# Optimization experiments

Measured on AMD Instinct MI355X. Metric: run time of the kernel, lower is better.

## Reference

```python
import jax, jax.numpy as jnp
import numpy as np

A, B, OBS, ACT, H, G = 8, 4096, 512, 64, 1024, 64
N, E = 10000, 40000
NODE, GH, NTYPES, AEMB = 32, 64, 8, 16


def _ln(x, g, b, eps=1e-5):
    m = jnp.mean(x, -1, keepdims=True)
    v = jnp.mean((x - m) ** 2, -1, keepdims=True)
    return (x - m) * jax.lax.rsqrt(v + eps) * g + b


def _neigh_mean(h, edges, n):
    # undirected mean aggregation: each dependency edge contributes both ways
    s, d = edges[:, 0], edges[:, 1]
    agg = jnp.zeros((n, h.shape[-1]), h.dtype).at[d].add(h[s]).at[s].add(h[d])
    deg = jnp.zeros((n,), h.dtype).at[d].add(1.0).at[s].add(1.0)
    return agg / jnp.maximum(deg, 1.0)[:, None]


def setup_inputs() -> dict:
    key = jax.random.key(0)
    ks = jax.random.split(key, 32)
    f32 = jnp.float32

    def w(k, i, o):
        return (jax.random.normal(k, (i, o), f32) / np.sqrt(i)).astype(f32)

    d = {}
    d["observations"] = jax.random.normal(ks[0], (A, B, OBS), f32)
    d["node_types"] = jax.random.randint(ks[1], (N,), 0, NTYPES)
    d["node_agents"] = jax.random.randint(ks[2], (N,), 0, A)
    d["edges"] = jax.random.randint(ks[3], (E, 2), 0, N)
    # graph encoder params
    d["type_embed"] = (jax.random.normal(ks[4], (NTYPES, NODE), f32) * 0.02).astype(f32)
    d["gagent_embed"] = (jax.random.normal(ks[5], (A, NODE), f32) * 0.02).astype(f32)
    d["W_l0"] = w(ks[6], 2 * NODE, GH); d["b_l0"] = jnp.zeros((GH,), f32)
    d["g_l0"] = jnp.ones((GH,), f32);   d["be_l0"] = jnp.zeros((GH,), f32)
    d["W_l1"] = w(ks[7], GH + GH, G);   d["b_l1"] = jnp.zeros((G,), f32)
    d["g_l1"] = jnp.ones((G,), f32);    d["be_l1"] = jnp.zeros((G,), f32)
    d["W_gp"] = w(ks[8], G, G);         d["b_gp"] = jnp.zeros((G,), f32)
    # shared policy params
    d["agent_embed"] = (jax.random.normal(ks[9], (A, AEMB), f32) * 0.02).astype(f32)
    d["Wp1"] = w(ks[10], OBS + G + AEMB, H); d["bp1"] = jnp.zeros((H,), f32)
    d["Wp2"] = w(ks[11], H, H);              d["bp2"] = jnp.zeros((H,), f32)
    d["Wp3"] = w(ks[12], H, ACT);            d["bp3"] = jnp.zeros((ACT,), f32)
    # value head params
    d["Wv1"] = w(ks[13], OBS * A + G, H); d["bv1"] = jnp.zeros((H,), f32)
    d["Wv2"] = w(ks[14], H, H);           d["bv2"] = jnp.zeros((H,), f32)
    d["Wv3"] = w(ks[15], H, 1);           d["bv3"] = jnp.zeros((1,), f32)
    return d


def _forward(observations, node_types, node_agents, edges,
             type_embed, gagent_embed, W_l0, b_l0, g_l0, be_l0,
             W_l1, b_l1, g_l1, be_l1, W_gp, b_gp,
             agent_embed, Wp1, bp1, Wp2, bp2, Wp3, bp3,
             Wv1, bv1, Wv2, bv2, Wv3, bv3):
    # --- graph encoder ---
    x = jnp.concatenate([type_embed[node_types], gagent_embed[node_agents]], -1)  # [N,64]
    # layer 0: aggregation is computed-but-ignored in the original; combined = x
    h = _ln(jax.nn.relu(x @ W_l0 + b_l0), g_l0, be_l0)                 # [N,GH]
    agg = _neigh_mean(h, edges, N)                                     # [N,GH]
    h = _ln(jax.nn.relu(jnp.concatenate([h, agg], -1) @ W_l1 + b_l1), g_l1, be_l1)  # [N,G]
    graph_embed = jnp.mean(h, 0) @ W_gp + b_gp                         # [G]

    ge = jnp.broadcast_to(graph_embed, (B, G))                         # [B,G]
    # --- shared policy over agents ---
    ae = jnp.broadcast_to(agent_embed[:, None, :], (A, B, AEMB))
    geA = jnp.broadcast_to(graph_embed, (A, B, G))
    comb = jnp.concatenate([observations, geA, ae], -1)                # [A,B,OBS+G+16]
    hp = jax.nn.relu(jnp.einsum("abi,io->abo", comb, Wp1) + bp1)
    hp = jax.nn.relu(jnp.einsum("abi,io->abo", hp, Wp2) + bp2)
    logits = jnp.einsum("abi,io->abo", hp, Wp3) + bp3                  # [A,B,ACT]
    # --- value head ---
    joint = jnp.transpose(observations, (1, 0, 2)).reshape(B, A * OBS)
    vin = jnp.concatenate([joint, ge], -1)                             # [B, A*OBS+G]
    hv = jax.nn.relu(vin @ Wv1 + bv1)
    hv = jax.nn.relu(hv @ Wv2 + bv2)
    value = hv @ Wv3 + bv3                                             # [B,1]
    return logits, value


def reference(observations, node_types, node_agents, edges,
              type_embed, gagent_embed, W_l0, b_l0, g_l0, be_l0,
              W_l1, b_l1, g_l1, be_l1, W_gp, b_gp,
              agent_embed, Wp1, bp1, Wp2, bp2, Wp3, bp3,
              Wv1, bv1, Wv2, bv2, Wv3, bv3):
    return _forward(observations, node_types, node_agents, edges,
                    type_embed, gagent_embed, W_l0, b_l0, g_l0, be_l0,
                    W_l1, b_l1, g_l1, be_l1, W_gp, b_gp,
                    agent_embed, Wp1, bp1, Wp2, bp2, Wp3, bp3,
                    Wv1, bv1, Wv2, bv2, Wv3, bv3)
```

## Files before the change

### kernel.cpp

```cpp
#include <hip/hip_runtime.h>
#include <hip/hip_bf16.h>

#define A_ 8
#define B_ 4096
#define OBS_ 512
#define ACT_ 64
#define H_ 1024
#define G_ 64
#define N_ 10000
#define E_ 40000

using bf16 = __hip_bfloat16;
typedef __attribute__((ext_vector_type(8))) short short8;
typedef __attribute__((ext_vector_type(4))) float f32x4;

__device__ __forceinline__ float wsum(float v) {
#pragma unroll
  for (int off = 32; off >= 1; off >>= 1) v += __shfl_xor(v, off, 64);
  return v;
}

__device__ __forceinline__ void storeC(float* p, float v) { *p = v; }
__device__ __forceinline__ void storeC(bf16* p, float v) { *p = __float2bfloat16(v); }

__device__ __forceinline__ unsigned short f2bu(float x) {
  bf16 h = __float2bfloat16(x);
  unsigned short u;
  __builtin_memcpy(&u, &h, 2);
  return u;
}

__device__ __forceinline__ void gload_lds16(const bf16* g, const void* lds_uniform) {
  __builtin_amdgcn_global_load_lds(
      (const __attribute__((address_space(1))) unsigned int*)g,
      (__attribute__((address_space(3))) unsigned int*)lds_uniform, 16, 0, 0);
}

template <int N>
__device__ __forceinline__ void waitvm() {
#define WV_CASE(n) if constexpr (N == n) asm volatile("s_waitcnt vmcnt(" #n ")" ::: "memory");
  WV_CASE(0) WV_CASE(1) WV_CASE(2) WV_CASE(3) WV_CASE(4) WV_CASE(5) WV_CASE(6) WV_CASE(7)
  WV_CASE(8) WV_CASE(9) WV_CASE(10) WV_CASE(12) WV_CASE(16)
  static_assert(N <= 16, "vmcnt too large");
#undef WV_CASE
}

__global__ __launch_bounds__(256) void prep_k(
    const float* __restrict__ obs, bf16* __restrict__ joint,
    const float* __restrict__ Wp1, bf16* __restrict__ Wp1t,
    const float* __restrict__ Wp2, bf16* __restrict__ Wp2t,
    const float* __restrict__ Wp3, bf16* __restrict__ Wp3t,
    const float* __restrict__ Wv1, bf16* __restrict__ Wv1t,
    const float* __restrict__ Wv2, bf16* __restrict__ Wv2t,
    const int* __restrict__ node_types, const int* __restrict__ node_agents,
    const float* __restrict__ type_embed, const float* __restrict__ gagent_embed,
    const float* __restrict__ W_l0, const float* __restrict__ b_l0,
    const float* __restrict__ g_l0, const float* __restrict__ be_l0,
    float* __restrict__ h0, float* __restrict__ agg, float* __restrict__ deg) {
  __shared__ float shb[32 * 33];
  const int bid = blockIdx.x, tid = threadIdx.x;
  if (bid < 8192) {
    size_t i = ((size_t)bid * 256 + tid) * 8;
    int a = (int)(i >> 21);
    int rem = (int)(i & ((1u << 21) - 1));
    int b = rem >> 9, k = rem & 511;
    const float* p = obs + i;
    short8 o;
#pragma unroll
    for (int t = 0; t < 8; t++) o[t] = (short)f2bu(p[t]);
    *(short8*)(joint + (size_t)b * 4096 + a * 512 + k) = o;
  } else if (bid < 14912) {
    int b = bid - 8192;
    const float* W;
    bf16* Wt;
    int K, N;
    if (b < 512) { W = Wp1; Wt = Wp1t; K = 512; N = 1024; }
    else if (b < 1536) { W = Wp2; Wt = Wp2t; K = 1024; N = 1024; b -= 512; }
    else if (b < 1600) { W = Wp3; Wt = Wp3t; K = 1024; N = 64; b -= 1536; }
    else if (b < 5696) { W = Wv1; Wt = Wv1t; K = 4096; N = 1024; b -= 1600; }
    else { W = Wv2; Wt = Wv2t; K = 1024; N = 1024; b -= 5696; }
    int nx = N >> 5;
    int n0 = (b % nx) * 32, k0 = (b / nx) * 32;
    int tx = tid & 31, ty = tid >> 5;
    float(*t2)[33] = (float(*)[33])shb;
#pragma unroll
    for (int r = ty; r < 32; r += 8) t2[r][tx] = W[(size_t)(k0 + r) * N + n0 + tx];
    __syncthreads();
#pragma unroll
    for (int r = ty; r < 32; r += 8)
      Wt[(size_t)(n0 + r) * K + k0 + tx] = __float2bfloat16(t2[tx][r]);
  } else {
    int nb = bid - 14912;
    int w = tid >> 6, t = tid & 63;
    int n = nb * 4 + w;
    float* xx = shb + w * 64;
    int ty2 = node_types[n], ag = node_agents[n];
    xx[t] = (t < 32) ? type_embed[ty2 * 32 + t] : gagent_embed[ag * 32 + (t - 32)];
    agg[(size_t)n * 64 + t] = 0.f;
    if (t == 0) deg[n] = 0.f;
    __syncthreads();
    float acc = b_l0[t];
#pragma unroll 8
    for (int i = 0; i < 64; i++) acc += xx[i] * W_l0[i * 64 + t];
    acc = fmaxf(acc, 0.f);
    float m = wsum(acc) * (1.f / 64.f);
    float d = acc - m;
    float v = wsum(d * d) * (1.f / 64.f);
    h0[(size_t)n * 64 + t] = d * rsqrtf(v + 1e-5f) * g_l0[t] + be_l0[t];
  }
}

__global__ void edge_k(const int* __restrict__ edges, const float* __restrict__ h0,
                       float* __restrict__ agg, float* __restrict__ deg) {
  int idx = blockIdx.x * 256 + threadIdx.x;
  if (idx >= E_ * 64) return;
  int e = idx >> 6, c = idx & 63;
  int s = edges[e * 2 + 0], d = edges[e * 2 + 1];
  atomicAdd(&agg[(size_t)d * 64 + c], h0[(size_t)s * 64 + c]);
  atomicAdd(&agg[(size_t)s * 64 + c], h0[(size_t)d * 64 + c]);
  if (c == 0) { atomicAdd(&deg[d], 1.f); atomicAdd(&deg[s], 1.f); }
}

__global__ __launch_bounds__(256) void gnn_l1_k(
    const float* __restrict__ h0, const float* __restrict__ agg, const float* __restrict__ deg,
    const float* __restrict__ W, const float* __restrict__ b, const float* __restrict__ g,
    const float* __restrict__ be, float* __restrict__ h1) {
  __shared__ float x[4][128];
  int w = threadIdx.x >> 6, t = threadIdx.x & 63;
  int n = blockIdx.x * 4 + w;
  x[w][t] = h0[(size_t)n * 64 + t];
  x[w][64 + t] = agg[(size_t)n * 64 + t] / fmaxf(deg[n], 1.0f);
  __syncthreads();
  float acc = b[t];
#pragma unroll 8
  for (int i = 0; i < 128; i++) acc += x[w][i] * W[i * 64 + t];
  acc = fmaxf(acc, 0.f);
  float m = wsum(acc) * (1.f / 64.f);
  float d = acc - m;
  float v = wsum(d * d) * (1.f / 64.f);
  h1[(size_t)n * 64 + t] = d * rsqrtf(v + 1e-5f) * g[t] + be[t];
}

__global__ void colmean_k(const float* __restrict__ h1, float* __restrict__ meanv) {
  int c = blockIdx.x, t = threadIdx.x;
  float s = 0.f;
  for (int n = t; n < N_; n += 256) s += h1[(size_t)n * 64 + c];
  __shared__ float red[256];
  red[t] = s;
  __syncthreads();
  for (int off = 128; off >= 1; off >>= 1) {
    if (t < off) red[t] += red[t + off];
    __syncthreads();
  }
  if (t == 0) meanv[c] = red[0] / (float)N_;
}

__global__ void fused_bias_k(const float* __restrict__ meanv, const float* __restrict__ Wgp,
                             const float* __restrict__ bgp, const float* __restrict__ agent_embed,
                             const float* __restrict__ Wp1, const float* __restrict__ bp1,
                             const float* __restrict__ Wv1, const float* __restrict__ bv1,
                             const float* __restrict__ bv3,
                             float* __restrict__ biasA, float* __restrict__ biasV,
                             float* __restrict__ value) {
  __shared__ float ge[64];
  int t = threadIdx.x;
  int gidx = blockIdx.x * 256 + t;
  if (gidx < B_) value[gidx] = bv3[0];
  if (t < 64) {
    float s = bgp[t];
    for (int g2 = 0; g2 < 64; g2++) s += meanv[g2] * Wgp[g2 * 64 + t];
    ge[t] = s;
  }
  __syncthreads();
  int blk = blockIdx.x;
  if (blk < 32) {
    int idx = blk * 256 + t;
    int a = idx >> 10, o = idx & 1023;
    float s = bp1[o];
    for (int g2 = 0; g2 < 64; g2++) s += ge[g2] * Wp1[(size_t)(512 + g2) * 1024 + o];
    for (int e = 0; e < 16; e++) s += agent_embed[a * 16 + e] * Wp1[(size_t)(576 + e) * 1024 + o];
    biasA[idx] = s;
  } else {
    int o = (blk - 32) * 256 + t;
    float s = bv1[o];
    for (int g2 = 0; g2 < 64; g2++) s += ge[g2] * Wv1[(size_t)(4096 + g2) * 1024 + o];
    biasV[o] = s;
  }
}

#define BARR()                        \
  asm volatile("" ::: "memory");      \
  __builtin_amdgcn_s_barrier();       \
  asm volatile("" ::: "memory")

#define RD8(off) (*(const short8*)(sb + (off)))

#define MMQ(FI0)                                                                     \
  __builtin_amdgcn_s_setprio(1);                                                     \
  acc[FI0 + 0][0] = __builtin_amdgcn_mfma_f32_16x16x32_bf16(a0, b0, acc[FI0 + 0][0], 0, 0, 0); \
  acc[FI0 + 0][1] = __builtin_amdgcn_mfma_f32_16x16x32_bf16(a0, b1, acc[FI0 + 0][1], 0, 0, 0); \
  acc[FI0 + 0][2] = __builtin_amdgcn_mfma_f32_16x16x32_bf16(a0, b2, acc[FI0 + 0][2], 0, 0, 0); \
  acc[FI0 + 0][3] = __builtin_amdgcn_mfma_f32_16x16x32_bf16(a0, b3, acc[FI0 + 0][3], 0, 0, 0); \
  acc[FI0 + 1][0] = __builtin_amdgcn_mfma_f32_16x16x32_bf16(a1, b0, acc[FI0 + 1][0], 0, 0, 0); \
  acc[FI0 + 1][1] = __builtin_amdgcn_mfma_f32_16x16x32_bf16(a1, b1, acc[FI0 + 1][1], 0, 0, 0); \
  acc[FI0 + 1][2] = __builtin_amdgcn_mfma_f32_16x16x32_bf16(a1, b2, acc[FI0 + 1][2], 0, 0, 0); \
  acc[FI0 + 1][3] = __builtin_amdgcn_mfma_f32_16x16x32_bf16(a1, b3, acc[FI0 + 1][3], 0, 0, 0); \
  acc[FI0 + 2][0] = __builtin_amdgcn_mfma_f32_16x16x32_bf16(a2, b0, acc[FI0 + 2][0], 0, 0, 0); \
  acc[FI0 + 2][1] = __builtin_amdgcn_mfma_f32_16x16x32_bf16(a2, b1, acc[FI0 + 2][1], 0, 0, 0); \
  acc[FI0 + 2][2] = __builtin_amdgcn_mfma_f32_16x16x32_bf16(a2, b2, acc[FI0 + 2][2], 0, 0, 0); \
  acc[FI0 + 2][3] = __builtin_amdgcn_mfma_f32_16x16x32_bf16(a2, b3, acc[FI0 + 2][3], 0, 0, 0); \
  acc[FI0 + 3][0] = __builtin_amdgcn_mfma_f32_16x16x32_bf16(a3, b0, acc[FI0 + 3][0], 0, 0, 0); \
  acc[FI0 + 3][1] = __builtin_amdgcn_mfma_f32_16x16x32_bf16(a3, b1, acc[FI0 + 3][1], 0, 0, 0); \
  acc[FI0 + 3][2] = __builtin_amdgcn_mfma_f32_16x16x32_bf16(a3, b2, acc[FI0 + 3][2], 0, 0, 0); \
  acc[FI0 + 3][3] = __builtin_amdgcn_mfma_f32_16x16x32_bf16(a3, b3, acc[FI0 + 3][3], 0, 0, 0); \
  __builtin_amdgcn_s_setprio(0)

template <int AMODE, int BIASMODE, bool RELU, typename TC>
__launch_bounds__(512, 1)
__global__ void g11_k(const bf16* __restrict__ Ap, const bf16* __restrict__ Bt,
                      const float* __restrict__ biasp, TC* __restrict__ Cp,
                      int M, int N, int K) {
  constexpr int SBUF = 65536;
  __shared__ char smem[2 * SBUF];

  const int tid = threadIdx.x;
  const int wid = tid >> 6, lane = tid & 63;
  const int wm = wid >> 2, wn = wid & 3;
  const int l15 = lane & 15;

  const int nwg = gridDim.x * gridDim.y;
  int fid = blockIdx.y * gridDim.x + blockIdx.x;
  int swz = (fid & 7) * (nwg >> 3) + (fid >> 3);
  const int m0 = (swz / gridDim.x) * 256;
  const int n0 = (swz % gridDim.x) * 256;

  f32x4 acc[8][4];
#pragma unroll
  for (int i = 0; i < 8; i++)
#pragma unroll
    for (int j = 0; j < 4; j++) acc[i][j] = (f32x4){0.f, 0.f, 0.f, 0.f};

  const bf16* pg[8];
  {
    int srow = tid >> 3;
    int c = (tid & 7) ^ (srow & 7);
#pragma unroll
    for (int g = 0; g < 4; ++g) {
      int r = m0 + g * 64 + srow;
      if (AMODE == 0)
        pg[g] = Ap + (size_t)r * K + c * 8;
      else
        pg[g] = Ap + (((size_t)(r & (B_ - 1))) << 12) + ((size_t)(r >> 12) << 9) + c * 8;
    }
#pragma unroll
    for (int g = 4; g < 8; ++g) {
      int r = n0 + (g - 4) * 64 + srow;
      pg[g] = Bt + (size_t)r * K + c * 8;
    }
  }

  const int slot0 = (lane >> 4) ^ (l15 & 7);
  const int aof0 = (wm * 128 + l15) * 128 + slot0 * 16;
  const int bof0 = 32768 + (wn * 64 + l15) * 128 + slot0 * 16;
  const int aof1 = aof0 ^ 64;
  const int bof1 = bof0 ^ 64;

#define STG(g, buf)                                                    \
  {                                                                    \
    gload_lds16(pg[g], smem + (buf) * SBUF + (g) * 8192 + wid * 1024); \
    pg[g] += 64;                                                       \
  }

  STG(0, 0) STG(2, 0) STG(4, 0) STG(5, 0) STG(6, 0) STG(7, 0) STG(1, 0) STG(3, 0)
  waitvm<0>();
  BARR();

  const int nt = K >> 6;
  for (int t = 0; t < nt; ++t) {
    const int cb = t & 1, ob = cb ^ 1;
    const bool last = (t == nt - 1);
    const char* sb = smem + cb * SBUF;
    short8 a0, a1, a2, a3, b0, b1, b2, b3;
    a0 = RD8(aof0 + 0 * 2048); a1 = RD8(aof0 + 1 * 2048);
    a2 = RD8(aof0 + 2 * 2048); a3 = RD8(aof0 + 3 * 2048);
    b0 = RD8(bof0 + 0 * 2048); b1 = RD8(bof0 + 1 * 2048);
    b2 = RD8(bof0 + 2 * 2048); b3 = RD8(bof0 + 3 * 2048);
    if (!last) { STG(0, ob) STG(2, ob) }
    BARR();
    MMQ(0);
    if (last) waitvm<0>(); else waitvm<2>();
    BARR();
    a0 = RD8(aof0 + 4 * 2048); a1 = RD8(aof0 + 5 * 2048);
    a2 = RD8(aof0 + 6 * 2048); a3 = RD8(aof0 + 7 * 2048);
    if (!last) { STG(4, ob) STG(5, ob) }
    BARR();
    MMQ(4);
    BARR();
    a0 = RD8(aof1 + 0 * 2048); a1 = RD8(aof1 + 1 * 2048);
    a2 = RD8(aof1 + 2 * 2048); a3 = RD8(aof1 + 3 * 2048);
    b0 = RD8(bof1 + 0 * 2048); b1 = RD8(bof1 + 1 * 2048);
    b2 = RD8(bof1 + 2 * 2048); b3 = RD8(bof1 + 3 * 2048);
    if (!last) { STG(6, ob) STG(7, ob) }
    BARR();
    MMQ(0);
    BARR();
    a0 = RD8(aof1 + 4 * 2048); a1 = RD8(aof1 + 5 * 2048);
    a2 = RD8(aof1 + 6 * 2048); a3 = RD8(aof1 + 7 * 2048);
    if (!last) { STG(1, ob) STG(3, ob) }
    BARR();
    MMQ(4);
    if (!last) waitvm<2>(); else waitvm<0>();
    BARR();
  }
#undef STG

#pragma unroll
  for (int i = 0; i < 8; ++i) {
    int rb = m0 + wm * 128 + i * 16 + (lane >> 4) * 4;
#pragma unroll
    for (int j = 0; j < 4; ++j) {
      int col = n0 + wn * 64 + j * 16 + l15;
#pragma unroll
      for (int r = 0; r < 4; r++) {
        int row = rb + r;
        float bias = (BIASMODE == 0) ? biasp[col] : biasp[((row >> 12) << 10) + col];
        float v = acc[i][j][r] + bias;
        if (RELU) v = fmaxf(v, 0.f);
        storeC(&Cp[(size_t)row * N + col], v);
      }
    }
  }
}

template <int FM, int FN, int WAVES_M, int WAVES_N, int DEPTH, int AMODE, int BIASMODE, bool RELU,
          typename TC, int VOUT>
__device__ void pgemm_dev(char* smem, const bf16* __restrict__ Ap, const bf16* __restrict__ Bt,
                          const float* __restrict__ biasp, TC* __restrict__ Cp,
                          int M, int N, int K, const float* __restrict__ Wv3,
                          float* __restrict__ vout, int fid, int gx, int nwg) {
  constexpr int NTHR = WAVES_M * WAVES_N * 64;
  constexpr int AR = WAVES_M * FM * 16;
  constexpr int BR = WAVES_N * FN * 16;
  constexpr int RPG = NTHR / 4;
  constexpr int AG = AR / RPG;
  constexpr int BG = BR / RPG;
  constexpr int G = AG + BG;
  constexpr int GRP = NTHR * 16;
  constexpr int ABYTES = AR * 64;
  constexpr int SBUF = (AR + BR) * 64;
  constexpr int NB = DEPTH + 1;

  const int tid = threadIdx.x;
  const int wid = tid >> 6, lane = tid & 63;
  const int wm = wid / WAVES_N, wn = wid % WAVES_N;
  const int l15 = lane & 15;

  int swz = (fid & 7) * (nwg >> 3) + (fid >> 3);
  const int m0 = (swz / gx) * AR;
  const int n0 = (swz % gx) * BR;

  f32x4 acc[FM][FN];
#pragma unroll
  for (int i = 0; i < FM; i++)
#pragma unroll
    for (int j = 0; j < FN; j++) acc[i][j] = (f32x4){0.f, 0.f, 0.f, 0.f};

  const bf16* pa[AG];
  const bf16* pb[BG];
  {
    int row = tid >> 2;
    int c = (tid & 3) ^ ((tid >> 3) & 3);
#pragma unroll
    for (int q = 0; q < AG; ++q) {
      int r = m0 + q * RPG + row;
      if (AMODE == 0)
        pa[q] = Ap + (size_t)r * K + c * 8;
      else
        pa[q] = Ap + (((size_t)(r & (B_ - 1))) << 12) + ((size_t)(r >> 12) << 9) + c * 8;
    }
#pragma unroll
    for (int q = 0; q < BG; ++q) {
      int r = n0 + q * RPG + row;
      pb[q] = Bt + (size_t)r * K + c * 8;
    }
  }

  const int cA = (lane >> 4) ^ ((l15 >> 1) & 3);
  const int offA0 = (wm * FM * 16 + l15) * 64 + cA * 16;
  const int offB0 = ABYTES + (wn * FN * 16 + l15) * 64 + cA * 16;

  auto stage = [&](int buf) {
    char* base = smem + buf * SBUF;
#pragma unroll
    for (int q = 0; q < AG; ++q) {
      gload_lds16(pa[q], base + q * GRP + wid * 1024);
      pa[q] += 32;
    }
#pragma unroll
    for (int q = 0; q < BG; ++q) {
      gload_lds16(pb[q], base + ABYTES + q * GRP + wid * 1024);
      pb[q] += 32;
    }
  };

  auto comp = [&](int buf) {
    const char* sb = smem + buf * SBUF;
    short8 bfr[FN];
#pragma unroll
    for (int j = 0; j < FN; ++j) bfr[j] = *(const short8*)(sb + offB0 + j * 1024);
    constexpr int FH = (FM > 4) ? FM / 2 : FM;
#pragma unroll
    for (int h = 0; h < FM / FH; ++h) {
      short8 afr[FH];
#pragma unroll
      for (int i = 0; i < FH; ++i) afr[i] = *(const short8*)(sb + offA0 + (h * FH + i) * 1024);
      __builtin_amdgcn_s_setprio(1);
#pragma unroll
      for (int i = 0; i < FH; ++i)
#pragma unroll
        for (int j = 0; j < FN; ++j)
          acc[h * FH + i][j] =
              __builtin_amdgcn_mfma_f32_16x16x32_bf16(afr[i], bfr[j], acc[h * FH + i][j], 0, 0, 0);
      __builtin_amdgcn_s_setprio(0);
    }
  };

  const int nt = K >> 5;
#pragma unroll
  for (int q = 0; q < DEPTH; ++q) stage(q);
  int cbuf = 0, sbi = DEPTH;
  for (int T = 0; T < nt - DEPTH; ++T) {
    stage(sbi);
    if (++sbi == NB) sbi = 0;
    waitvm<DEPTH * G>();
    __builtin_amdgcn_s_barrier();
    asm volatile("" ::: "memory");
    comp(cbuf);
    if (++cbuf == NB) cbuf = 0;
    asm volatile("" ::: "memory");
    __builtin_amdgcn_s_barrier();
  }
#define DRAIN(d)                       \
  {                                    \
    waitvm<(d) * G>();                 \
    __builtin_amdgcn_s_barrier();      \
    asm volatile("" ::: "memory");     \
    comp(cbuf);                        \
    if (++cbuf == NB) cbuf = 0;        \
    asm volatile("" ::: "memory");     \
  }
  if constexpr (DEPTH == 4) { DRAIN(3) DRAIN(2) }
  DRAIN(1)
  DRAIN(0)
#undef DRAIN

#pragma unroll
  for (int i = 0; i < FM; ++i) {
    int rb = m0 + wm * FM * 16 + i * 16 + (lane >> 4) * 4;
    if constexpr (VOUT) {
#pragma unroll
      for (int r = 0; r < 4; r++) {
        int row = rb + r;
        float s = 0.f;
#pragma unroll
        for (int j = 0; j < FN; ++j) {
          int col = n0 + wn * FN * 16 + j * 16 + l15;
          float v = acc[i][j][r] + biasp[col];
          if (RELU) v = fmaxf(v, 0.f);
          s += v * Wv3[col];
        }
        s += __shfl_xor(s, 1, 64);
        s += __shfl_xor(s, 2, 64);
        s += __shfl_xor(s, 4, 64);
        s += __shfl_xor(s, 8, 64);
        if (l15 == 0) atomicAdd(&vout[row], s);
      }
    } else {
#pragma unroll
      for (int j = 0; j < FN; ++j) {
        int col = n0 + wn * FN * 16 + j * 16 + l15;
#pragma unroll
        for (int r = 0; r < 4; r++) {
          int row = rb + r;
          float bias = (BIASMODE == 0) ? biasp[col] : biasp[((row >> 12) << 10) + col];
          float v = acc[i][j][r] + bias;
          if (RELU) v = fmaxf(v, 0.f);
          storeC(&Cp[(size_t)row * N + col], v);
        }
      }
    }
  }
}

template <int FM, int FN, int WAVES_M, int WAVES_N, int DEPTH, int AMODE, int BIASMODE, bool RELU,
          typename TC, int VOUT = 0>
__launch_bounds__(WAVES_M * WAVES_N * 64, 2)
__global__ void pgemm_k(const bf16* __restrict__ Ap, const bf16* __restrict__ Bt,
                        const float* __restrict__ biasp, TC* __restrict__ Cp,
                        int M, int N, int K,
                        const float* __restrict__ Wv3 = nullptr,
                        float* __restrict__ vout = nullptr) {
  constexpr int SBUF = ((WAVES_M * FM * 16) + (WAVES_N * FN * 16)) * 64;
  __shared__ char smem[(DEPTH + 1) * SBUF];
  int fid = blockIdx.y * gridDim.x + blockIdx.x;
  pgemm_dev<FM, FN, WAVES_M, WAVES_N, DEPTH, AMODE, BIASMODE, RELU, TC, VOUT>(
      smem, Ap, Bt, biasp, Cp, M, N, K, Wv3, vout, fid, gridDim.x, gridDim.x * gridDim.y);
}

__launch_bounds__(256, 2)
__global__ void pv_k(const bf16* __restrict__ C2, const bf16* __restrict__ Wp3t,
                     const float* __restrict__ bp3, float* __restrict__ logits,
                     const bf16* __restrict__ hv, const bf16* __restrict__ Wv2t,
                     const float* __restrict__ bv2, const float* __restrict__ Wv3,
                     float* __restrict__ value) {
  __shared__ char smem[49152];
  if (blockIdx.x < 256) {
    pgemm_dev<4, 2, 2, 2, 2, 0, 0, false, float, 0>(
        smem, C2, Wp3t, bp3, logits, 32768, 64, 1024, nullptr, nullptr, blockIdx.x, 1, 256);
  } else {
    pgemm_dev<4, 4, 2, 2, 2, 0, 0, true, bf16, 1>(
        smem, hv, Wv2t, bv2, (bf16*)nullptr, 4096, 1024, 1024, Wv3, value, blockIdx.x - 256, 8,
        256);
  }
}

extern "C" void kernel_launch(void* const* d_in, const int* in_sizes, int n_in,
                              void* d_out, int out_size, void* d_ws, size_t ws_size,
                              hipStream_t stream) {
  const float* obs = (const float*)d_in[0];
  const int* node_types = (const int*)d_in[1];
  const int* node_agents = (const int*)d_in[2];
  const int* edges = (const int*)d_in[3];
  const float* type_embed = (const float*)d_in[4];
  const float* gagent_embed = (const float*)d_in[5];
  const float* W_l0 = (const float*)d_in[6];
  const float* b_l0 = (const float*)d_in[7];
  const float* g_l0 = (const float*)d_in[8];
  const float* be_l0 = (const float*)d_in[9];
  const float* W_l1 = (const float*)d_in[10];
  const float* b_l1 = (const float*)d_in[11];
  const float* g_l1 = (const float*)d_in[12];
  const float* be_l1 = (const float*)d_in[13];
  const float* W_gp = (const float*)d_in[14];
  const float* b_gp = (const float*)d_in[15];
  const float* agent_embed = (const float*)d_in[16];
  const float* Wp1 = (const float*)d_in[17];
  const float* bp1 = (const float*)d_in[18];
  const float* Wp2 = (const float*)d_in[19];
  const float* bp2 = (const float*)d_in[20];
  const float* Wp3 = (const float*)d_in[21];
  const float* bp3 = (const float*)d_in[22];
  const float* Wv1 = (const float*)d_in[23];
  const float* bv1 = (const float*)d_in[24];
  const float* Wv2 = (const float*)d_in[25];
  const float* bv2 = (const float*)d_in[26];
  const float* Wv3 = (const float*)d_in[27];
  const float* bv3 = (const float*)d_in[28];

  char* wsp = (char*)d_ws;
  auto alloc = [&](size_t bytes) {
    char* p = wsp;
    wsp += (bytes + 255) & ~(size_t)255;
    return p;
  };
  float* h0 = (float*)alloc((size_t)N_ * 64 * 4);
  float* agg = (float*)alloc((size_t)N_ * 64 * 4);
  float* deg = (float*)alloc((size_t)N_ * 4);
  float* h1 = (float*)alloc((size_t)N_ * 64 * 4);
  float* meanv = (float*)alloc(64 * 4);
  float* biasA = (float*)alloc(8 * 1024 * 4);
  float* biasV = (float*)alloc(1024 * 4);
  bf16* joint = (bf16*)alloc((size_t)4096 * 4096 * 2);
  bf16* Wp1t = (bf16*)alloc((size_t)1024 * 512 * 2);
  bf16* Wp2t = (bf16*)alloc((size_t)1024 * 1024 * 2);
  bf16* Wp3t = (bf16*)alloc((size_t)64 * 1024 * 2);
  bf16* Wv1t = (bf16*)alloc((size_t)1024 * 4096 * 2);
  bf16* Wv2t = (bf16*)alloc((size_t)1024 * 1024 * 2);
  bf16* C1 = (bf16*)alloc((size_t)32768 * 1024 * 2);
  bf16* C2 = (bf16*)alloc((size_t)32768 * 1024 * 2);
  bf16* hv = (bf16*)alloc((size_t)4096 * 1024 * 2);

  float* logits = (float*)d_out;
  float* value = (float*)d_out + (size_t)A_ * B_ * ACT_;

  prep_k<<<17412, 256, 0, stream>>>(obs, joint, Wp1, Wp1t, Wp2, Wp2t, Wp3, Wp3t, Wv1, Wv1t, Wv2,
                                    Wv2t, node_types, node_agents, type_embed, gagent_embed, W_l0,
                                    b_l0, g_l0, be_l0, h0, agg, deg);
  edge_k<<<(E_ * 64) / 256, 256, 0, stream>>>(edges, h0, agg, deg);
  gnn_l1_k<<<N_ / 4, 256, 0, stream>>>(h0, agg, deg, W_l1, b_l1, g_l1, be_l1, h1);
  colmean_k<<<64, 256, 0, stream>>>(h1, meanv);
  fused_bias_k<<<36, 256, 0, stream>>>(meanv, W_gp, b_gp, agent_embed, Wp1, bp1, Wv1, bv1, bv3,
                                       biasA, biasV, value);

  g11_k<1, 1, true, bf16>
      <<<dim3(4, 128), 512, 0, stream>>>(joint, Wp1t, biasA, C1, 32768, 1024, 512);
  g11_k<0, 0, true, bf16>
      <<<dim3(4, 128), 512, 0, stream>>>(C1, Wp2t, bp2, C2, 32768, 1024, 1024);
  pgemm_k<4, 4, 2, 2, 2, 0, 0, true, bf16>
      <<<dim3(8, 32), 256, 0, stream>>>(joint, Wv1t, biasV, hv, 4096, 1024, 4096);
  pv_k<<<512, 256, 0, stream>>>(C2, Wp3t, bp3, logits, hv, Wv2t, bv2, Wv3, value);
}
```

Before: 272.7 us.

## Fuse policy-L1 and value-L1 GEMMs into one launch; fold column mean into GNN layer

```diff
diff --git a/kernel.cpp b/kernel.cpp
--- a/kernel.cpp
+++ b/kernel.cpp
@@ -111,7 +111,9 @@
 }
 
 __global__ void edge_k(const int* __restrict__ edges, const float* __restrict__ h0,
-                       float* __restrict__ agg, float* __restrict__ deg) {
+                       float* __restrict__ agg, float* __restrict__ deg,
+                       float* __restrict__ colsum) {
+  if (blockIdx.x == 0 && threadIdx.x < 64) colsum[threadIdx.x] = 0.f;
   int idx = blockIdx.x * 256 + threadIdx.x;
   if (idx >= E_ * 64) return;
   int e = idx >> 6, c = idx & 63;
@@ -124,7 +126,7 @@
 __global__ __launch_bounds__(256) void gnn_l1_k(
     const float* __restrict__ h0, const float* __restrict__ agg, const float* __restrict__ deg,
     const float* __restrict__ W, const float* __restrict__ b, const float* __restrict__ g,
-    const float* __restrict__ be, float* __restrict__ h1) {
+    const float* __restrict__ be, float* __restrict__ h1, float* __restrict__ colsum) {
   __shared__ float x[4][128];
   int w = threadIdx.x >> 6, t = threadIdx.x & 63;
   int n = blockIdx.x * 4 + w;
@@ -138,24 +140,15 @@
   float m = wsum(acc) * (1.f / 64.f);
   float d = acc - m;
   float v = wsum(d * d) * (1.f / 64.f);
-  h1[(size_t)n * 64 + t] = d * rsqrtf(v + 1e-5f) * g[t] + be[t];
-}
-
-__global__ void colmean_k(const float* __restrict__ h1, float* __restrict__ meanv) {
-  int c = blockIdx.x, t = threadIdx.x;
-  float s = 0.f;
-  for (int n = t; n < N_; n += 256) s += h1[(size_t)n * 64 + c];
-  __shared__ float red[256];
-  red[t] = s;
+  float out = d * rsqrtf(v + 1e-5f) * g[t] + be[t];
+  h1[(size_t)n * 64 + t] = out;
   __syncthreads();
-  for (int off = 128; off >= 1; off >>= 1) {
-    if (t < off) red[t] += red[t + off];
-    __syncthreads();
-  }
-  if (t == 0) meanv[c] = red[0] / (float)N_;
-}
-
-__global__ void fused_bias_k(const float* __restrict__ meanv, const float* __restrict__ Wgp,
+  x[w][t] = out;
+  __syncthreads();
+  if (w == 0) atomicAdd(&colsum[t], x[0][t] + x[1][t] + x[2][t] + x[3][t]);
+}
+
+__global__ void fused_bias_k(const float* __restrict__ colsum, const float* __restrict__ Wgp,
                              const float* __restrict__ bgp, const float* __restrict__ agent_embed,
                              const float* __restrict__ Wp1, const float* __restrict__ bp1,
                              const float* __restrict__ Wv1, const float* __restrict__ bv1,
@@ -168,7 +161,7 @@
   if (gidx < B_) value[gidx] = bv3[0];
   if (t < 64) {
     float s = bgp[t];
-    for (int g2 = 0; g2 < 64; g2++) s += meanv[g2] * Wgp[g2 * 64 + t];
+    for (int g2 = 0; g2 < 64; g2++) s += (colsum[g2] * (1.f / (float)N_)) * Wgp[g2 * 64 + t];
     ge[t] = s;
   }
   __syncthreads();
@@ -215,121 +208,110 @@
   acc[FI0 + 3][3] = __builtin_amdgcn_mfma_f32_16x16x32_bf16(a3, b3, acc[FI0 + 3][3], 0, 0, 0); \
   __builtin_amdgcn_s_setprio(0)
 
+#define G11_BODY(AMODE, BIASMODE, RELU, TC, Ap, Bt, biasp, Cp, M, N, K, fid, gx, nwg)           \
+  {                                                                                             \
+    constexpr int SBUF = 65536;                                                                 \
+    const int tid = threadIdx.x;                                                                \
+    const int wid = tid >> 6, lane = tid & 63;                                                  \
+    const int wm = wid >> 2, wn = wid & 3;                                                      \
+    const int l15 = lane & 15;                                                                  \
+    int swz = ((fid) & 7) * ((nwg) >> 3) + ((fid) >> 3);                                        \
+    const int m0 = (swz / (gx)) * 256;                                                          \
+    const int n0 = (swz % (gx)) * 256;                                                          \
+    f32x4 acc[8][4];                                                                            \
+    _Pragma("unroll") for (int i = 0; i < 8; i++)                                               \
+        _Pragma("unroll") for (int j = 0; j < 4; j++) acc[i][j] = (f32x4){0.f, 0.f, 0.f, 0.f};  \
+    const bf16* pg[8];                                                                          \
+    {                                                                                           \
+      int srow = tid >> 3;                                                                      \
+      int c = (tid & 7) ^ (srow & 7);                                                           \
+      _Pragma("unroll") for (int g = 0; g < 4; ++g) {                                           \
+        int r = m0 + g * 64 + srow;                                                             \
+        if (AMODE == 0)                                                                         \
+          pg[g] = (Ap) + (size_t)r * (K) + c * 8;                                               \
+        else                                                                                    \
+          pg[g] = (Ap) + (((size_t)(r & (B_ - 1))) << 12) + ((size_t)(r >> 12) << 9) + c * 8;   \
+      }                                                                                         \
+      _Pragma("unroll") for (int g = 4; g < 8; ++g) {                                           \
+        int r = n0 + (g - 4) * 64 + srow;                                                       \
+        pg[g] = (Bt) + (size_t)r * (K) + c * 8;                                                 \
+      }                                                                                         \
+    }                                                                                           \
+    const int slot0 = (lane >> 4) ^ (l15 & 7);                                                  \
+    const int aof0 = (wm * 128 + l15) * 128 + slot0 * 16;                                       \
+    const int bof0 = 32768 + (wn * 64 + l15) * 128 + slot0 * 16;                                \
+    const int aof1 = aof0 ^ 64;                                                                 \
+    const int bof1 = bof0 ^ 64;                                                                 \
+    STG(0, 0) STG(2, 0) STG(4, 0) STG(5, 0) STG(6, 0) STG(7, 0) STG(1, 0) STG(3, 0)            \
+    waitvm<0>();                                                                                \
+    BARR();                                                                                     \
+    const int nt = (K) >> 6;                                                                    \
+    for (int t = 0; t < nt; ++t) {                                                              \
+      const int cb = t & 1, ob = cb ^ 1;                                                        \
+      const bool last = (t == nt - 1);                                                          \
+      const char* sb = smem + cb * SBUF;                                                        \
+      short8 a0, a1, a2, a3, b0, b1, b2, b3;                                                    \
+      a0 = RD8(aof0 + 0 * 2048); a1 = RD8(aof0 + 1 * 2048);                                     \
+      a2 = RD8(aof0 + 2 * 2048); a3 = RD8(aof0 + 3 * 2048);                                     \
+      b0 = RD8(bof0 + 0 * 2048); b1 = RD8(bof0 + 1 * 2048);                                     \
+      b2 = RD8(bof0 + 2 * 2048); b3 = RD8(bof0 + 3 * 2048);                                     \
+      if (!last) { STG(0, ob) STG(2, ob) }                                                      \
+      BARR();                                                                                   \
+      MMQ(0);                                                                                   \
+      if (last) waitvm<0>(); else waitvm<2>();                                                  \
+      BARR();                                                                                   \
+      a0 = RD8(aof0 + 4 * 2048); a1 = RD8(aof0 + 5 * 2048);                                     \
+      a2 = RD8(aof0 + 6 * 2048); a3 = RD8(aof0 + 7 * 2048);                                     \
+      if (!last) { STG(4, ob) STG(5, ob) }                                                      \
+      BARR();                                                                                   \
+      MMQ(4);                                                                                   \
+      BARR();                                                                                   \
+      a0 = RD8(aof1 + 0 * 2048); a1 = RD8(aof1 + 1 * 2048);                                     \
+      a2 = RD8(aof1 + 2 * 2048); a3 = RD8(aof1 + 3 * 2048);                                     \
+      b0 = RD8(bof1 + 0 * 2048); b1 = RD8(bof1 + 1 * 2048);                                     \
+      b2 = RD8(bof1 + 2 * 2048); b3 = RD8(bof1 + 3 * 2048);                                     \
+      if (!last) { STG(6, ob) STG(7, ob) }                                                      \
+      BARR();                                                                                   \
+      MMQ(0);                                                                                   \
+      BARR();                                                                                   \
+      a0 = RD8(aof1 + 4 * 2048); a1 = RD8(aof1 + 5 * 2048);                                     \
+      a2 = RD8(aof1 + 6 * 2048); a3 = RD8(aof1 + 7 * 2048);                                     \
+      if (!last) { STG(1, ob) STG(3, ob) }                                                      \
+      BARR();                                                                                   \
+      MMQ(4);                                                                                   \
+      if (!last) waitvm<2>(); else waitvm<0>();                                                 \
+      BARR();                                                                                   \
+    }                                                                                           \
+    _Pragma("unroll") for (int i = 0; i < 8; ++i) {                                             \
+      int rb = m0 + wm * 128 + i * 16 + (lane >> 4) * 4;                                        \
+      _Pragma("unroll") for (int j = 0; j < 4; ++j) {                                           \
+        int col = n0 + wn * 64 + j * 16 + l15;                                                  \
+        _Pragma("unroll") for (int r = 0; r < 4; r++) {                                         \
+          int row = rb + r;                                                                     \
+          float bias = (BIASMODE == 0) ? (biasp)[col] : (biasp)[((row >> 12) << 10) + col];     \
+          float v = acc[i][j][r] + bias;                                                        \
+          if (RELU) v = fmaxf(v, 0.f);                                                          \
+          storeC(&(Cp)[(size_t)row * (N) + col], v);                                            \
+        }                                                                                       \
+      }                                                                                         \
+    }                                                                                           \
+  }
+
+#define STG(g, buf)                                                    \
+  {                                                                    \
+    gload_lds16(pg[g], smem + (buf) * 65536 + (g) * 8192 + wid * 1024); \
+    pg[g] += 64;                                                       \
+  }
+
 template <int AMODE, int BIASMODE, bool RELU, typename TC>
 __launch_bounds__(512, 1)
 __global__ void g11_k(const bf16* __restrict__ Ap, const bf16* __restrict__ Bt,
                       const float* __restrict__ biasp, TC* __restrict__ Cp,
                       int M, int N, int K) {
-  constexpr int SBUF = 65536;
-  __shared__ char smem[2 * SBUF];
-
-  const int tid = threadIdx.x;
-  const int wid = tid >> 6, lane = tid & 63;
-  const int wm = wid >> 2, wn = wid & 3;
-  const int l15 = lane & 15;
-
-  const int nwg = gridDim.x * gridDim.y;
+  __shared__ char smem[131072];
   int fid = blockIdx.y * gridDim.x + blockIdx.x;
-  int swz = (fid & 7) * (nwg >> 3) + (fid >> 3);
-  const int m0 = (swz / gridDim.x) * 256;
-  const int n0 = (swz % gridDim.x) * 256;
-
-  f32x4 acc[8][4];
-#pragma unroll
-  for (int i = 0; i < 8; i++)
-#pragma unroll
-    for (int j = 0; j < 4; j++) acc[i][j] = (f32x4){0.f, 0.f, 0.f, 0.f};
-
-  const bf16* pg[8];
-  {
-    int srow = tid >> 3;
-    int c = (tid & 7) ^ (srow & 7);
-#pragma unroll
-    for (int g = 0; g < 4; ++g) {
-      int r = m0 + g * 64 + srow;
-      if (AMODE == 0)
-        pg[g] = Ap + (size_t)r * K + c * 8;
-      else
-        pg[g] = Ap + (((size_t)(r & (B_ - 1))) << 12) + ((size_t)(r >> 12) << 9) + c * 8;
-    }
-#pragma unroll
-    for (int g = 4; g < 8; ++g) {
-      int r = n0 + (g - 4) * 64 + srow;
-      pg[g] = Bt + (size_t)r * K + c * 8;
-    }
-  }
-
-  const int slot0 = (lane >> 4) ^ (l15 & 7);
-  const int aof0 = (wm * 128 + l15) * 128 + slot0 * 16;
-  const int bof0 = 32768 + (wn * 64 + l15) * 128 + slot0 * 16;
-  const int aof1 = aof0 ^ 64;
-  const int bof1 = bof0 ^ 64;
-
-#define STG(g, buf)                                                    \
-  {                                                                    \
-    gload_lds16(pg[g], smem + (buf) * SBUF + (g) * 8192 + wid * 1024); \
-    pg[g] += 64;                                                       \
-  }
-
-  STG(0, 0) STG(2, 0) STG(4, 0) STG(5, 0) STG(6, 0) STG(7, 0) STG(1, 0) STG(3, 0)
-  waitvm<0>();
-  BARR();
-
-  const int nt = K >> 6;
-  for (int t = 0; t < nt; ++t) {
-    const int cb = t & 1, ob = cb ^ 1;
-    const bool last = (t == nt - 1);
-    const char* sb = smem + cb * SBUF;
-    short8 a0, a1, a2, a3, b0, b1, b2, b3;
-    a0 = RD8(aof0 + 0 * 2048); a1 = RD8(aof0 + 1 * 2048);
-    a2 = RD8(aof0 + 2 * 2048); a3 = RD8(aof0 + 3 * 2048);
-    b0 = RD8(bof0 + 0 * 2048); b1 = RD8(bof0 + 1 * 2048);
-    b2 = RD8(bof0 + 2 * 2048); b3 = RD8(bof0 + 3 * 2048);
-    if (!last) { STG(0, ob) STG(2, ob) }
-    BARR();
-    MMQ(0);
-    if (last) waitvm<0>(); else waitvm<2>();
-    BARR();
-    a0 = RD8(aof0 + 4 * 2048); a1 = RD8(aof0 + 5 * 2048);
-    a2 = RD8(aof0 + 6 * 2048); a3 = RD8(aof0 + 7 * 2048);
-    if (!last) { STG(4, ob) STG(5, ob) }
-    BARR();
-    MMQ(4);
-    BARR();
-    a0 = RD8(aof1 + 0 * 2048); a1 = RD8(aof1 + 1 * 2048);
-    a2 = RD8(aof1 + 2 * 2048); a3 = RD8(aof1 + 3 * 2048);
-    b0 = RD8(bof1 + 0 * 2048); b1 = RD8(bof1 + 1 * 2048);
-    b2 = RD8(bof1 + 2 * 2048); b3 = RD8(bof1 + 3 * 2048);
-    if (!last) { STG(6, ob) STG(7, ob) }
-    BARR();
-    MMQ(0);
-    BARR();
-    a0 = RD8(aof1 + 4 * 2048); a1 = RD8(aof1 + 5 * 2048);
-    a2 = RD8(aof1 + 6 * 2048); a3 = RD8(aof1 + 7 * 2048);
-    if (!last) { STG(1, ob) STG(3, ob) }
-    BARR();
-    MMQ(4);
-    if (!last) waitvm<2>(); else waitvm<0>();
-    BARR();
-  }
-#undef STG
-
-#pragma unroll
-  for (int i = 0; i < 8; ++i) {
-    int rb = m0 + wm * 128 + i * 16 + (lane >> 4) * 4;
-#pragma unroll
-    for (int j = 0; j < 4; ++j) {
-      int col = n0 + wn * 64 + j * 16 + l15;
-#pragma unroll
-      for (int r = 0; r < 4; r++) {
-        int row = rb + r;
-        float bias = (BIASMODE == 0) ? biasp[col] : biasp[((row >> 12) << 10) + col];
-        float v = acc[i][j][r] + bias;
-        if (RELU) v = fmaxf(v, 0.f);
-        storeC(&Cp[(size_t)row * N + col], v);
-      }
-    }
-  }
+  G11_BODY(AMODE, BIASMODE, RELU, TC, Ap, Bt, biasp, Cp, M, N, K, fid, gridDim.x,
+           gridDim.x * gridDim.y)
 }
 
 template <int FM, int FN, int WAVES_M, int WAVES_N, int DEPTH, int AMODE, int BIASMODE, bool RELU,
@@ -492,19 +474,20 @@
   }
 }
 
-template <int FM, int FN, int WAVES_M, int WAVES_N, int DEPTH, int AMODE, int BIASMODE, bool RELU,
-          typename TC, int VOUT = 0>
-__launch_bounds__(WAVES_M * WAVES_N * 64, 2)
-__global__ void pgemm_k(const bf16* __restrict__ Ap, const bf16* __restrict__ Bt,
-                        const float* __restrict__ biasp, TC* __restrict__ Cp,
-                        int M, int N, int K,
-                        const float* __restrict__ Wv3 = nullptr,
-                        float* __restrict__ vout = nullptr) {
-  constexpr int SBUF = ((WAVES_M * FM * 16) + (WAVES_N * FN * 16)) * 64;
-  __shared__ char smem[(DEPTH + 1) * SBUF];
-  int fid = blockIdx.y * gridDim.x + blockIdx.x;
-  pgemm_dev<FM, FN, WAVES_M, WAVES_N, DEPTH, AMODE, BIASMODE, RELU, TC, VOUT>(
-      smem, Ap, Bt, biasp, Cp, M, N, K, Wv3, vout, fid, gridDim.x, gridDim.x * gridDim.y);
+__launch_bounds__(512, 1)
+__global__ void pv1_k(const bf16* __restrict__ joint, const bf16* __restrict__ Wp1t,
+                      const float* __restrict__ biasA, bf16* __restrict__ C1,
+                      const bf16* __restrict__ Wv1t, const float* __restrict__ biasV,
+                      bf16* __restrict__ hv) {
+  __shared__ char smem[131072];
+  if (blockIdx.x < 512) {
+    int fid = blockIdx.x;
+    G11_BODY(1, 1, true, bf16, joint, Wp1t, biasA, C1, 32768, 1024, 512, fid, 4, 512)
+  } else {
+    pgemm_dev<4, 2, 2, 4, 2, 0, 0, true, bf16, 0>(
+        smem, joint, Wv1t, biasV, hv, 4096, 1024, 4096, nullptr, nullptr, (int)blockIdx.x - 512,
+        8, 256);
+  }
 }
 
 __launch_bounds__(256, 2)
@@ -567,7 +550,7 @@
   float* agg = (float*)alloc((size_t)N_ * 64 * 4);
   float* deg = (float*)alloc((size_t)N_ * 4);
   float* h1 = (float*)alloc((size_t)N_ * 64 * 4);
-  float* meanv = (float*)alloc(64 * 4);
+  float* colsum = (float*)alloc(64 * 4);
   float* biasA = (float*)alloc(8 * 1024 * 4);
   float* biasV = (float*)alloc(1024 * 4);
   bf16* joint = (bf16*)alloc((size_t)4096 * 4096 * 2);
@@ -586,17 +569,13 @@
   prep_k<<<17412, 256, 0, stream>>>(obs, joint, Wp1, Wp1t, Wp2, Wp2t, Wp3, Wp3t, Wv1, Wv1t, Wv2,
                                     Wv2t, node_types, node_agents, type_embed, gagent_embed, W_l0,
                                     b_l0, g_l0, be_l0, h0, agg, deg);
-  edge_k<<<(E_ * 64) / 256, 256, 0, stream>>>(edges, h0, agg, deg);
-  gnn_l1_k<<<N_ / 4, 256, 0, stream>>>(h0, agg, deg, W_l1, b_l1, g_l1, be_l1, h1);
-  colmean_k<<<64, 256, 0, stream>>>(h1, meanv);
-  fused_bias_k<<<36, 256, 0, stream>>>(meanv, W_gp, b_gp, agent_embed, Wp1, bp1, Wv1, bv1, bv3,
+  edge_k<<<(E_ * 64) / 256, 256, 0, stream>>>(edges, h0, agg, deg, colsum);
+  gnn_l1_k<<<N_ / 4, 256, 0, stream>>>(h0, agg, deg, W_l1, b_l1, g_l1, be_l1, h1, colsum);
+  fused_bias_k<<<36, 256, 0, stream>>>(colsum, W_gp, b_gp, agent_embed, Wp1, bp1, Wv1, bv1, bv3,
                                        biasA, biasV, value);
 
-  g11_k<1, 1, true, bf16>
-      <<<dim3(4, 128), 512, 0, stream>>>(joint, Wp1t, biasA, C1, 32768, 1024, 512);
+  pv1_k<<<768, 512, 0, stream>>>(joint, Wp1t, biasA, C1, Wv1t, biasV, hv);
   g11_k<0, 0, true, bf16>
       <<<dim3(4, 128), 512, 0, stream>>>(C1, Wp2t, bp2, C2, 32768, 1024, 1024);
-  pgemm_k<4, 4, 2, 2, 2, 0, 0, true, bf16>
-      <<<dim3(8, 32), 256, 0, stream>>>(joint, Wv1t, biasV, hv, 4096, 1024, 4096);
   pv_k<<<512, 256, 0, stream>>>(C2, Wp3t, bp3, logits, hv, Wv2t, bv2, Wv3, value);
 }
```

After: 308.5 us. 13.1% more time.
